# Kernel optimization log

Measured on AMD Instinct MI355X. Metric: run time of the kernel, lower is better.

The kernel has to match this reference:

```python
import jax, jax.numpy as jnp
import numpy as np

OVERSAMP = 2


def _pad_last2(x, H2, W2):
    # centered zero-pad of last two dims to (H2, W2) -- PadLast
    H, W = x.shape[-2], x.shape[-1]
    ph, pw = (H2 - H) // 2, (W2 - W) // 2
    pad = [(0, 0)] * (x.ndim - 2) + [(ph, H2 - H - ph), (pw, W2 - W - pw)]
    return jnp.pad(x, pad)


def _crop_last2(x, H, W):
    # centered crop of last two dims to (H, W) -- PadLast.adjoint
    H2, W2 = x.shape[-2], x.shape[-1]
    ph, pw = (H2 - H) // 2, (W2 - W) // 2
    return x[..., ph:ph + H, pw:pw + W]


def setup_inputs() -> dict:
    key = jax.random.key(0)
    ks = jax.random.split(key, 6)
    A, C, H, W = 5, 12, 256, 256
    Hp, Wp = OVERSAMP * H, OVERSAMP * W
    x_r = jax.random.normal(ks[0], (A, H, W), dtype=jnp.float32)
    x_i = jax.random.normal(ks[1], (A, H, W), dtype=jnp.float32)
    mps_r = jax.random.normal(ks[2], (C, H, W), dtype=jnp.float32) * 0.1
    mps_i = jax.random.normal(ks[3], (C, H, W), dtype=jnp.float32) * 0.1
    kern_r = jax.random.normal(ks[4], (A, A, Hp, Wp), dtype=jnp.float32) * 0.1
    kern_i = jax.random.normal(ks[5], (A, A, Hp, Wp), dtype=jnp.float32) * 0.1
    return {"x_r": x_r, "x_i": x_i, "mps_r": mps_r, "mps_i": mps_i,
            "kern_r": kern_r, "kern_i": kern_i}


def reference(x_r, x_i, mps_r, mps_i, kern_r, kern_i):
    # Toeplitz normal operator AHA_func: x [A,H,W] -> [A,H,W]
    x = jax.lax.complex(x_r, x_i)          # [A,H,W]
    mps = jax.lax.complex(mps_r, mps_i)    # [C,H,W]
    kernels = jax.lax.complex(kern_r, kern_i)  # [Aout,Ain,2H,2W]
    A, H, W = x.shape
    Hp, Wp = kernels.shape[-2], kernels.shape[-1]
    # coil modulation: x[None,:] * mps[:,None] -> [C,A,H,W]
    cx = mps[:, None, :, :] * x[None, :, :, :]
    cx = _pad_last2(cx, Hp, Wp)            # [C,A,2H,2W]
    Fx = jnp.fft.fftn(cx, axes=(-2, -1), norm='ortho')
    # Fx[:,None] [C,1,Ain,2H,2W] * kernels [Aout,Ain,2H,2W] -> [C,Aout,Ain,2H,2W]
    y = (OVERSAMP ** 2) * jnp.fft.ifftn(Fx[:, None, ...] * kernels,
                                        axes=(-2, -1), norm='ortho')
    y = jnp.sum(y, axis=2)                 # sum over Ain -> [C,Aout,2H,2W]
    y = _crop_last2(y, H, W)               # [C,A,H,W]
    y = y * jnp.conj(mps)[:, None, :, :]
    return jnp.sum(y, axis=0)              # [A,H,W]
```

## Files before the change

### kernel.cpp

```cpp
#include <hip/hip_runtime.h>
#include <cstddef>

#define A_  5
#define C_  12
#define RPG (C_ * A_)
#define TWO_PI 6.28318530717958647692f
#define NPAD 596

__device__ float2 g_bufA[RPG * 512 * 256];
__device__ float2 g_bufB[RPG * 512 * 256];

__device__ __forceinline__ int P5(int i) { return i + 5 * (i >> 5); }
__device__ __forceinline__ int PT(int i) { return i + (i >> 3); }

__device__ __forceinline__ void build_tab(float2* tab, int t) {
    #pragma unroll
    for (int q = 0; q < 2; ++q) {
        int k = t + q * 128;
        float s, c;
        __sincosf(-TWO_PI * (float)k * (1.0f / 512.0f), &s, &c);
        tab[PT(k)] = make_float2(c, s);
    }
}

template<int DIR>
__device__ __forceinline__ float2 cmulw(float2 v, float2 w) {
    float cv = w.x, sv = (DIR < 0) ? w.y : -w.y;
    return make_float2(v.x * cv - v.y * sv, v.x * sv + v.y * cv);
}

template<int DIR, int NB>
__device__ void fftB(float (*AR)[NPAD], float (*AI)[NPAD],
                     float (*BR)[NPAD], float (*BI)[NPAD],
                     const float2* tab, int t) {
    float (*sR)[NPAD] = AR; float (*sI)[NPAD] = AI;
    float (*dR)[NPAD] = BR; float (*dI)[NPAD] = BI;
    int Ns = 1;
    #pragma unroll
    for (int s = 0; s < 4; ++s) {
        __syncthreads();
        int m = t & (Ns - 1);
        int e1 = m << (7 - 2 * s);
        float2 w1 = tab[PT(e1)], w2 = tab[PT(2 * e1)];
        float2 w3 = make_float2(w1.x * w2.x - w1.y * w2.y,
                                w1.x * w2.y + w1.y * w2.x);
        int i0 = P5(t), i1 = P5(t + 128), i2 = P5(t + 256), i3 = P5(t + 384);
        int idxD = ((t & ~(Ns - 1)) << 2) | m;
        int o0 = P5(idxD), o1 = P5(idxD + Ns);
        int o2 = P5(idxD + 2 * Ns), o3 = P5(idxD + 3 * Ns);
        #pragma unroll
        for (int b = 0; b < NB; ++b) {
            float2 v0 = make_float2(sR[b][i0], sI[b][i0]);
            float2 v1 = cmulw<DIR>(make_float2(sR[b][i1], sI[b][i1]), w1);
            float2 v2 = cmulw<DIR>(make_float2(sR[b][i2], sI[b][i2]), w2);
            float2 v3 = cmulw<DIR>(make_float2(sR[b][i3], sI[b][i3]), w3);
            float2 t0 = make_float2(v0.x + v2.x, v0.y + v2.y);
            float2 t1 = make_float2(v0.x - v2.x, v0.y - v2.y);
            float2 t2 = make_float2(v1.x + v3.x, v1.y + v3.y);
            float2 t3 = make_float2(v1.x - v3.x, v1.y - v3.y);
            float2 y0 = make_float2(t0.x + t2.x, t0.y + t2.y);
            float2 y2 = make_float2(t0.x - t2.x, t0.y - t2.y);
            float2 y1, y3;
            if (DIR < 0) {
                y1 = make_float2(t1.x + t3.y, t1.y - t3.x);
                y3 = make_float2(t1.x - t3.y, t1.y + t3.x);
            } else {
                y1 = make_float2(t1.x - t3.y, t1.y + t3.x);
                y3 = make_float2(t1.x + t3.y, t1.y - t3.x);
            }
            dR[b][o0] = y0.x; dI[b][o0] = y0.y;
            dR[b][o1] = y1.x; dI[b][o1] = y1.y;
            dR[b][o2] = y2.x; dI[b][o2] = y2.y;
            dR[b][o3] = y3.x; dI[b][o3] = y3.y;
        }
        { auto tp = sR; sR = dR; dR = tp; }
        { auto tp = sI; sI = dI; dI = tp; }
        Ns <<= 2;
    }
    __syncthreads();
    #pragma unroll
    for (int q = 0; q < 2; ++q) {
        int j2 = t + q * 128;
        float2 w = tab[PT(j2)];
        int i0 = P5(j2), i1 = P5(j2 + 256);
        #pragma unroll
        for (int b = 0; b < NB; ++b) {
            float2 v0 = make_float2(sR[b][i0], sI[b][i0]);
            float2 tw = cmulw<DIR>(make_float2(sR[b][i1], sI[b][i1]), w);
            dR[b][i0] = v0.x + tw.x; dI[b][i0] = v0.y + tw.y;
            dR[b][i1] = v0.x - tw.x; dI[b][i1] = v0.y - tw.y;
        }
    }
    __syncthreads();
}

__global__ void k_zero(float* __restrict__ out, int n) {
    int i = blockIdx.x * 256 + threadIdx.x;
    int stride = gridDim.x * 256;
    for (; i < n; i += stride) out[i] = 0.f;
}

__global__ void __launch_bounds__(128) k_fft1c(const float* __restrict__ xr_,
        const float* __restrict__ xi_, const float* __restrict__ mr_,
        const float* __restrict__ mi_) {
    __shared__ float AR[4][NPAD], AI[4][NPAD], BR[4][NPAD], BI[4][NPAD];
    __shared__ float2 tab[288];
    int bid = blockIdx.x;
    int ca = bid >> 6;
    int x0 = (bid & 63) << 2;
    int coil = ca / A_, a = ca % A_;
    int t = threadIdx.x;
    build_tab(tab, t);
    int xc = t & 3, yo = t >> 2;
    int xcol = x0 + xc;
    const float* xr = xr_ + a * 65536;
    const float* xi = xi_ + a * 65536;
    const float* mr = mr_ + coil * 65536;
    const float* mi = mi_ + coil * 65536;
    #pragma unroll
    for (int r = 0; r < 4; ++r) {
        int z = yo + 32 * r;
        AR[xc][P5(z)] = 0.f;        AI[xc][P5(z)] = 0.f;
        AR[xc][P5(384 + z)] = 0.f;  AI[xc][P5(384 + z)] = 0.f;
    }
    #pragma unroll
    for (int r = 0; r < 8; ++r) {
        int y = yo + 32 * r;
        int idx = y * 256 + xcol;
        float xrv = xr[idx], xiv = xi[idx], mrv = mr[idx], miv = mi[idx];
        int p = P5(128 + y);
        AR[xc][p] = xrv * mrv - xiv * miv;
        AI[xc][p] = xrv * miv + xiv * mrv;
    }
    fftB<-1, 4>(AR, AI, BR, BI, tab, t);
    float2* o = g_bufA + (size_t)ca * 131072 + x0 + xc;
    #pragma unroll
    for (int rr = 0; rr < 16; ++rr) {
        int ky = yo + 32 * rr;
        int p = P5(ky);
        o[(size_t)ky * 256] = make_float2(BR[xc][p], BI[xc][p]);
    }
}

#define KLOAD(KR, KI, q) { _Pragma("unroll")                                   \
    for (int m = 0; m < 25; ++m) {                                             \
        size_t idx = ((size_t)m << 18) + kyBase + (size_t)(t + (q) * 128);     \
        KR[m] = kr[idx]; KI[m] = ki[idx]; } }

#define MIXQ(KR, KI, q) { int p = P5(t + (q) * 128);                           \
    float fr[5], fi[5];                                                        \
    _Pragma("unroll") for (int ain = 0; ain < 5; ++ain) {                      \
        fr[ain] = F1R[ain][p]; fi[ain] = F1I[ain][p]; }                        \
    _Pragma("unroll") for (int ao = 0; ao < 5; ++ao) {                         \
        float gr = 0.f, gi = 0.f;                                              \
        _Pragma("unroll") for (int ain = 0; ain < 5; ++ain) {                  \
            float kre = KR[ao * 5 + ain], kim = KI[ao * 5 + ain];              \
            gr += kre * fr[ain] - kim * fi[ain];                               \
            gi += kre * fi[ain] + kim * fr[ain]; }                             \
        F1R[ao][p] = scale * gr; F1I[ao][p] = scale * gi; } }

__global__ void __launch_bounds__(128) k_colfmc(const float* __restrict__ kr,
                                                const float* __restrict__ ki) {
    __shared__ float F0R[5][NPAD], F0I[5][NPAD], F1R[5][NPAD], F1I[5][NPAD];
    __shared__ float2 tab[288];
    int b = blockIdx.x;
    int xcd = b & 7, s = b >> 3;
    int v = s / 96, wv = s % 96;
    int u = xcd + (v << 3);
    int coil = wv % C_;
    int ky = (u << 3) + (wv / C_);
    int t = threadIdx.x;
    build_tab(tab, t);
    const float2* bA = g_bufA + (size_t)(coil * A_) * 131072 + ((size_t)ky << 8);
    float4 row[5];
    #pragma unroll
    for (int ain = 0; ain < 5; ++ain)
        row[ain] = ((const float4*)(bA + (size_t)ain * 131072))[t];
    size_t kyBase = (size_t)ky << 9;
    float kRa[25], kIa[25], kRb[25], kIb[25];
    KLOAD(kRa, kIa, 0);
    #pragma unroll
    for (int ain = 0; ain < 5; ++ain) {
        F0R[ain][P5(t)] = 0.f;        F0I[ain][P5(t)] = 0.f;
        F0R[ain][P5(t + 384)] = 0.f;  F0I[ain][P5(t + 384)] = 0.f;
        int p0 = P5(128 + 2 * t), p1 = P5(129 + 2 * t);
        F0R[ain][p0] = row[ain].x; F0I[ain][p0] = row[ain].y;
        F0R[ain][p1] = row[ain].z; F0I[ain][p1] = row[ain].w;
    }
    fftB<-1, 5>(F0R, F0I, F1R, F1I, tab, t);
    const float scale = 4.0f / 262144.0f;
    KLOAD(kRb, kIb, 1);
    MIXQ(kRa, kIa, 0);
    KLOAD(kRa, kIa, 2);
    MIXQ(kRb, kIb, 1);
    KLOAD(kRb, kIb, 3);
    MIXQ(kRa, kIa, 2);
    MIXQ(kRb, kIb, 3);
    fftB<1, 5>(F1R, F1I, F0R, F0I, tab, t);
    #pragma unroll
    for (int ao = 0; ao < 5; ++ao) {
        int p0 = P5(128 + 2 * t), p1 = P5(129 + 2 * t);
        float4 vv = make_float4(F0R[ao][p0], F0I[ao][p0],
                                F0R[ao][p1], F0I[ao][p1]);
        ((float4*)(g_bufB + (size_t)(coil * A_ + ao) * 131072 +
                   ((size_t)ky << 8)))[t] = vv;
    }
}

__global__ void __launch_bounds__(128) k_outfr(const float* __restrict__ mr_,
        const float* __restrict__ mi_, float* __restrict__ out, int outFloats) {
    __shared__ float AR[4][NPAD], AI[4][NPAD], BR[4][NPAD], BI[4][NPAD];
    __shared__ float2 tab[288];
    int bid = blockIdx.x;
    int a = bid >> 8;
    int x0 = ((bid >> 2) & 63) << 2;
    int cg = bid & 3;
    int t = threadIdx.x;
    build_tab(tab, t);
    int xc = t & 3, yo = t >> 2;
    int xcol = x0 + xc;
    float accR[8], accI[8];
    #pragma unroll
    for (int r = 0; r < 8; ++r) { accR[r] = 0.f; accI[r] = 0.f; }
    for (int cc = 0; cc < 3; ++cc) {
        int c = cg * 3 + cc;
        const float2* src = g_bufB + (size_t)(c * A_ + a) * 131072 + xcol;
        #pragma unroll
        for (int rr = 0; rr < 16; ++rr) {
            int ky = yo + 32 * rr;
            float2 vv = src[(size_t)ky * 256];
            int p = P5(ky);
            AR[xc][p] = vv.x; AI[xc][p] = vv.y;
        }
        fftB<1, 4>(AR, AI, BR, BI, tab, t);
        const float* mr = mr_ + c * 65536;
        const float* mi = mi_ + c * 65536;
        #pragma unroll
        for (int rr = 0; rr < 8; ++rr) {
            int y = yo + 32 * rr;
            int p = P5(128 + y);
            float vx = BR[xc][p], vy = BI[xc][p];
            int idx = y * 256 + xcol;
            float mrv = mr[idx], miv = mi[idx];
            accR[rr] += vx * mrv + vy * miv;
            accI[rr] += vy * mrv - vx * miv;
        }
    }
    #pragma unroll
    for (int rr = 0; rr < 8; ++rr) {
        int y = yo + 32 * rr;
        size_t r0 = (size_t)a * 65536 + (size_t)y * 256 + xcol;
        size_t i0 = 327680 + r0;
        if (r0 < (size_t)outFloats) atomicAdd(&out[r0], accR[rr]);
        if (i0 < (size_t)outFloats) atomicAdd(&out[i0], accI[rr]);
    }
}

extern "C" void kernel_launch(void* const* d_in, const int* in_sizes, int n_in,
                              void* d_out, int out_size, void* d_ws, size_t ws_size,
                              hipStream_t stream) {
    const float* xr = (const float*)d_in[0];
    const float* xi = (const float*)d_in[1];
    const float* mr = (const float*)d_in[2];
    const float* mi = (const float*)d_in[3];
    const float* kr = (const float*)d_in[4];
    const float* ki = (const float*)d_in[5];
    float* out = (float*)d_out;
    (void)d_ws; (void)ws_size; (void)n_in; (void)in_sizes;

    int nz = out_size < 655360 ? out_size : 655360;
    k_zero  <<<256, 256, 0, stream>>>(out, nz);
    k_fft1c <<<RPG * 64, 128, 0, stream>>>(xr, xi, mr, mi);
    k_colfmc<<<C_ * 512, 128, 0, stream>>>(kr, ki);
    k_outfr <<<A_ * 256, 128, 0, stream>>>(mr, mi, out, out_size);
}
```

Baseline: 313.3 us.

## Use wavefront-local radix-8 FFT in mix kernel and double threads per block

The middle kernel's row FFTs become a per-wavefront 512-point radix-8 transform held in registers. Each of five wavefronts does one channel and exchanges data through LDS with only s_waitcnt instead of block barriers. The kernel-matrix mixing now loads kernel values inline across 256 threads instead of prefetching into large register arrays. The column FFT kernels move from 128 to 256 threads, each thread handling two of the four columns, to raise parallelism and cut per-thread work. This trades fewer barriers and less register pressure for twiddles computed by recurrence, which lose some accuracy, and for less overlap of the kernel loads.

```diff
diff --git a/kernel.cpp b/kernel.cpp
--- a/kernel.cpp
+++ b/kernel.cpp
@@ -13,13 +13,11 @@
 __device__ __forceinline__ int P5(int i) { return i + 5 * (i >> 5); }
 __device__ __forceinline__ int PT(int i) { return i + (i >> 3); }
 
-__device__ __forceinline__ void build_tab(float2* tab, int t) {
-    #pragma unroll
-    for (int q = 0; q < 2; ++q) {
-        int k = t + q * 128;
+__device__ __forceinline__ void build_tab256(float2* tab, int t) {
+    if (t < 256) {
         float s, c;
-        __sincosf(-TWO_PI * (float)k * (1.0f / 512.0f), &s, &c);
-        tab[PT(k)] = make_float2(c, s);
+        __sincosf(-TWO_PI * (float)t * (1.0f / 512.0f), &s, &c);
+        tab[PT(t)] = make_float2(c, s);
     }
 }
 
@@ -29,27 +27,100 @@
     return make_float2(v.x * cv - v.y * sv, v.x * sv + v.y * cv);
 }
 
-template<int DIR, int NB>
-__device__ void fftB(float (*AR)[NPAD], float (*AI)[NPAD],
-                     float (*BR)[NPAD], float (*BI)[NPAD],
-                     const float2* tab, int t) {
+template<int DIR>
+__device__ __forceinline__ void dft8(float* xr, float* xi) {
+    const float S = 0.70710678118654752f;
+    float ar[4], ai[4], br[4], bi[4];
+#pragma unroll
+    for (int j = 0; j < 4; ++j) {
+        ar[j] = xr[j] + xr[j+4]; ai[j] = xi[j] + xi[j+4];
+        br[j] = xr[j] - xr[j+4]; bi[j] = xi[j] - xi[j+4];
+    }
+    float t;
+    if (DIR < 0) {
+        t = S*(br[1]+bi[1]); bi[1] = S*(bi[1]-br[1]); br[1] = t;
+        t = bi[2];           bi[2] = -br[2];          br[2] = t;
+        t = S*(bi[3]-br[3]); bi[3] = -S*(br[3]+bi[3]); br[3] = t;
+    } else {
+        t = S*(br[1]-bi[1]); bi[1] = S*(bi[1]+br[1]); br[1] = t;
+        t = -bi[2];          bi[2] = br[2];           br[2] = t;
+        t = -S*(br[3]+bi[3]); bi[3] = S*(br[3]-bi[3]); br[3] = t;
+    }
+    float c0r=ar[0]+ar[2], c0i=ai[0]+ai[2], c1r=ar[1]+ar[3], c1i=ai[1]+ai[3];
+    float d0r=ar[0]-ar[2], d0i=ai[0]-ai[2], d1r, d1i;
+    if (DIR < 0) { d1r =  ai[1]-ai[3]; d1i = -(ar[1]-ar[3]); }
+    else         { d1r = -(ai[1]-ai[3]); d1i =  ar[1]-ar[3]; }
+    xr[0]=c0r+c1r; xi[0]=c0i+c1i; xr[4]=c0r-c1r; xi[4]=c0i-c1i;
+    xr[2]=d0r+d1r; xi[2]=d0i+d1i; xr[6]=d0r-d1r; xi[6]=d0i-d1i;
+    c0r=br[0]+br[2]; c0i=bi[0]+bi[2]; c1r=br[1]+br[3]; c1i=bi[1]+bi[3];
+    d0r=br[0]-br[2]; d0i=bi[0]-bi[2];
+    if (DIR < 0) { d1r =  bi[1]-bi[3]; d1i = -(br[1]-br[3]); }
+    else         { d1r = -(bi[1]-bi[3]); d1i =  br[1]-br[3]; }
+    xr[1]=c0r+c1r; xi[1]=c0i+c1i; xr[5]=c0r-c1r; xi[5]=c0i-c1i;
+    xr[3]=d0r+d1r; xi[3]=d0i+d1i; xr[7]=d0r-d1r; xi[7]=d0i-d1i;
+}
+
+__device__ __forceinline__ void twiddle_chain(float* vr, float* vi, float ang) {
+    float s, c; __sincosf(ang, &s, &c);
+    float twr = c, twi = s;
+#pragma unroll
+    for (int d = 1; d < 8; ++d) {
+        float tr = vr[d]*twr - vi[d]*twi;
+        vi[d]    = vr[d]*twi + vi[d]*twr;
+        vr[d]    = tr;
+        float nr = twr*c - twi*s;
+        twi      = twr*s + twi*c;
+        twr      = nr;
+    }
+}
+
+template<int DIR>
+__device__ __forceinline__ void wfft512(float* vr, float* vi,
+                                        float* sre, float* sim, int lh) {
+    const float sgn = (DIR < 0) ? -1.f : 1.f;
+    dft8<DIR>(vr, vi);
+    twiddle_chain(vr, vi, sgn * (TWO_PI/512.f) * (float)lh);
+#pragma unroll
+    for (int d = 0; d < 8; ++d) { sre[72*d+lh] = vr[d]; sim[72*d+lh] = vi[d]; }
+    asm volatile("s_waitcnt lgkmcnt(0)" ::: "memory");
+    int rb = 72*(lh>>3) + (lh&7);
+#pragma unroll
+    for (int e = 0; e < 8; ++e) { vr[e] = sre[rb+8*e]; vi[e] = sim[rb+8*e]; }
+    dft8<DIR>(vr, vi);
+    twiddle_chain(vr, vi, sgn * (TWO_PI/64.f) * (float)(lh & 7));
+    int wb = 9*(lh>>3) + (lh&7);
+#pragma unroll
+    for (int h = 0; h < 8; ++h) { sre[72*h+wb] = vr[h]; sim[72*h+wb] = vi[h]; }
+    asm volatile("s_waitcnt lgkmcnt(0)" ::: "memory");
+    int rb2 = 72*(lh&7) + 9*(lh>>3);
+#pragma unroll
+    for (int f = 0; f < 8; ++f) { vr[f] = sre[rb2+f]; vi[f] = sim[rb2+f]; }
+    dft8<DIR>(vr, vi);
+}
+
+template<int DIR>
+__device__ void fftB4(float (*AR)[NPAD], float (*AI)[NPAD],
+                      float (*BR)[NPAD], float (*BI)[NPAD],
+                      const float2* tab, int t) {
+    int tt = t & 127, b0 = (t >> 7) << 1;
     float (*sR)[NPAD] = AR; float (*sI)[NPAD] = AI;
     float (*dR)[NPAD] = BR; float (*dI)[NPAD] = BI;
     int Ns = 1;
     #pragma unroll
     for (int s = 0; s < 4; ++s) {
         __syncthreads();
-        int m = t & (Ns - 1);
+        int m = tt & (Ns - 1);
         int e1 = m << (7 - 2 * s);
         float2 w1 = tab[PT(e1)], w2 = tab[PT(2 * e1)];
         float2 w3 = make_float2(w1.x * w2.x - w1.y * w2.y,
                                 w1.x * w2.y + w1.y * w2.x);
-        int i0 = P5(t), i1 = P5(t + 128), i2 = P5(t + 256), i3 = P5(t + 384);
-        int idxD = ((t & ~(Ns - 1)) << 2) | m;
+        int i0 = P5(tt), i1 = P5(tt + 128), i2 = P5(tt + 256), i3 = P5(tt + 384);
+        int idxD = ((tt & ~(Ns - 1)) << 2) | m;
         int o0 = P5(idxD), o1 = P5(idxD + Ns);
         int o2 = P5(idxD + 2 * Ns), o3 = P5(idxD + 3 * Ns);
         #pragma unroll
-        for (int b = 0; b < NB; ++b) {
+        for (int bb = 0; bb < 2; ++bb) {
+            int b = b0 + bb;
             float2 v0 = make_float2(sR[b][i0], sI[b][i0]);
             float2 v1 = cmulw<DIR>(make_float2(sR[b][i1], sI[b][i1]), w1);
             float2 v2 = cmulw<DIR>(make_float2(sR[b][i2], sI[b][i2]), w2);
@@ -80,11 +151,12 @@
     __syncthreads();
     #pragma unroll
     for (int q = 0; q < 2; ++q) {
-        int j2 = t + q * 128;
+        int j2 = tt + q * 128;
         float2 w = tab[PT(j2)];
         int i0 = P5(j2), i1 = P5(j2 + 256);
         #pragma unroll
-        for (int b = 0; b < NB; ++b) {
+        for (int bb = 0; bb < 2; ++bb) {
+            int b = b0 + bb;
             float2 v0 = make_float2(sR[b][i0], sI[b][i0]);
             float2 tw = cmulw<DIR>(make_float2(sR[b][i1], sI[b][i1]), w);
             dR[b][i0] = v0.x + tw.x; dI[b][i0] = v0.y + tw.y;
@@ -100,7 +172,7 @@
     for (; i < n; i += stride) out[i] = 0.f;
 }
 
-__global__ void __launch_bounds__(128) k_fft1c(const float* __restrict__ xr_,
+__global__ void __launch_bounds__(256) k_fft1c(const float* __restrict__ xr_,
         const float* __restrict__ xi_, const float* __restrict__ mr_,
         const float* __restrict__ mi_) {
     __shared__ float AR[4][NPAD], AI[4][NPAD], BR[4][NPAD], BI[4][NPAD];
@@ -110,7 +182,7 @@
     int x0 = (bid & 63) << 2;
     int coil = ca / A_, a = ca % A_;
     int t = threadIdx.x;
-    build_tab(tab, t);
+    build_tab256(tab, t);
     int xc = t & 3, yo = t >> 2;
     int xcol = x0 + xc;
     const float* xr = xr_ + a * 65536;
@@ -118,51 +190,34 @@
     const float* mr = mr_ + coil * 65536;
     const float* mi = mi_ + coil * 65536;
     #pragma unroll
-    for (int r = 0; r < 4; ++r) {
-        int z = yo + 32 * r;
+    for (int r = 0; r < 2; ++r) {
+        int z = yo + 64 * r;
         AR[xc][P5(z)] = 0.f;        AI[xc][P5(z)] = 0.f;
         AR[xc][P5(384 + z)] = 0.f;  AI[xc][P5(384 + z)] = 0.f;
     }
     #pragma unroll
-    for (int r = 0; r < 8; ++r) {
-        int y = yo + 32 * r;
+    for (int r = 0; r < 4; ++r) {
+        int y = yo + 64 * r;
         int idx = y * 256 + xcol;
         float xrv = xr[idx], xiv = xi[idx], mrv = mr[idx], miv = mi[idx];
         int p = P5(128 + y);
         AR[xc][p] = xrv * mrv - xiv * miv;
         AI[xc][p] = xrv * miv + xiv * mrv;
     }
-    fftB<-1, 4>(AR, AI, BR, BI, tab, t);
+    fftB4<-1>(AR, AI, BR, BI, tab, t);
     float2* o = g_bufA + (size_t)ca * 131072 + x0 + xc;
     #pragma unroll
-    for (int rr = 0; rr < 16; ++rr) {
-        int ky = yo + 32 * rr;
+    for (int rr = 0; rr < 8; ++rr) {
+        int ky = yo + 64 * rr;
         int p = P5(ky);
         o[(size_t)ky * 256] = make_float2(BR[xc][p], BI[xc][p]);
     }
 }
 
-#define KLOAD(KR, KI, q) { _Pragma("unroll")                                   \
-    for (int m = 0; m < 25; ++m) {                                             \
-        size_t idx = ((size_t)m << 18) + kyBase + (size_t)(t + (q) * 128);     \
-        KR[m] = kr[idx]; KI[m] = ki[idx]; } }
-
-#define MIXQ(KR, KI, q) { int p = P5(t + (q) * 128);                           \
-    float fr[5], fi[5];                                                        \
-    _Pragma("unroll") for (int ain = 0; ain < 5; ++ain) {                      \
-        fr[ain] = F1R[ain][p]; fi[ain] = F1I[ain][p]; }                        \
-    _Pragma("unroll") for (int ao = 0; ao < 5; ++ao) {                         \
-        float gr = 0.f, gi = 0.f;                                              \
-        _Pragma("unroll") for (int ain = 0; ain < 5; ++ain) {                  \
-            float kre = KR[ao * 5 + ain], kim = KI[ao * 5 + ain];              \
-            gr += kre * fr[ain] - kim * fi[ain];                               \
-            gi += kre * fi[ain] + kim * fr[ain]; }                             \
-        F1R[ao][p] = scale * gr; F1I[ao][p] = scale * gi; } }
-
-__global__ void __launch_bounds__(128) k_colfmc(const float* __restrict__ kr,
+__global__ void __launch_bounds__(320) k_colfmc(const float* __restrict__ kr,
                                                 const float* __restrict__ ki) {
-    __shared__ float F0R[5][NPAD], F0I[5][NPAD], F1R[5][NPAD], F1I[5][NPAD];
-    __shared__ float2 tab[288];
+    __shared__ float FRe[A_][512], FIm[A_][512];
+    __shared__ float shR[A_][576], shI[A_][576];
     int b = blockIdx.x;
     int xcd = b & 7, s = b >> 3;
     int v = s / 96, wv = s % 96;
@@ -170,44 +225,79 @@
     int coil = wv % C_;
     int ky = (u << 3) + (wv / C_);
     int t = threadIdx.x;
-    build_tab(tab, t);
-    const float2* bA = g_bufA + (size_t)(coil * A_) * 131072 + ((size_t)ky << 8);
-    float4 row[5];
-    #pragma unroll
-    for (int ain = 0; ain < 5; ++ain)
-        row[ain] = ((const float4*)(bA + (size_t)ain * 131072))[t];
-    size_t kyBase = (size_t)ky << 9;
-    float kRa[25], kIa[25], kRb[25], kIb[25];
-    KLOAD(kRa, kIa, 0);
-    #pragma unroll
-    for (int ain = 0; ain < 5; ++ain) {
-        F0R[ain][P5(t)] = 0.f;        F0I[ain][P5(t)] = 0.f;
-        F0R[ain][P5(t + 384)] = 0.f;  F0I[ain][P5(t + 384)] = 0.f;
-        int p0 = P5(128 + 2 * t), p1 = P5(129 + 2 * t);
-        F0R[ain][p0] = row[ain].x; F0I[ain][p0] = row[ain].y;
-        F0R[ain][p1] = row[ain].z; F0I[ain][p1] = row[ain].w;
-    }
-    fftB<-1, 5>(F0R, F0I, F1R, F1I, tab, t);
+    int w = t >> 6, L = t & 63;
+    int sig = ((L & 7) << 3) | (L >> 3);
+    float* sre = shR[w]; float* sim = shI[w];
+
+    {
+        const float2* row = g_bufA + (size_t)(coil * A_ + w) * 131072 +
+                            ((size_t)ky << 8);
+        float vr[8], vi[8];
+        #pragma unroll
+        for (int r = 0; r < 8; ++r) { vr[r] = 0.f; vi[r] = 0.f; }
+        #pragma unroll
+        for (int r = 2; r < 6; ++r) {
+            float2 vv = row[((r - 2) << 6) + L];
+            vr[r] = vv.x; vi[r] = vv.y;
+        }
+        wfft512<-1>(vr, vi, sre, sim, L);
+        #pragma unroll
+        for (int g = 0; g < 8; ++g) {
+            int kx = (g << 6) + sig;
+            FRe[w][kx] = vr[g]; FIm[w][kx] = vi[g];
+        }
+    }
+    __syncthreads();
+
     const float scale = 4.0f / 262144.0f;
-    KLOAD(kRb, kIb, 1);
-    MIXQ(kRa, kIa, 0);
-    KLOAD(kRa, kIa, 2);
-    MIXQ(kRb, kIb, 1);
-    KLOAD(kRb, kIb, 3);
-    MIXQ(kRa, kIa, 2);
-    MIXQ(kRb, kIb, 3);
-    fftB<1, 5>(F1R, F1I, F0R, F0I, tab, t);
-    #pragma unroll
-    for (int ao = 0; ao < 5; ++ao) {
-        int p0 = P5(128 + 2 * t), p1 = P5(129 + 2 * t);
-        float4 vv = make_float4(F0R[ao][p0], F0I[ao][p0],
-                                F0R[ao][p1], F0I[ao][p1]);
-        ((float4*)(g_bufB + (size_t)(coil * A_ + ao) * 131072 +
-                   ((size_t)ky << 8)))[t] = vv;
-    }
-}
-
-__global__ void __launch_bounds__(128) k_outfr(const float* __restrict__ mr_,
+    if (t < 256) {
+        size_t kyb = (size_t)ky << 9;
+        #pragma unroll
+        for (int h = 0; h < 2; ++h) {
+            int kx = t + (h << 8);
+            float fr[A_], fi[A_];
+            #pragma unroll
+            for (int ain = 0; ain < A_; ++ain) {
+                fr[ain] = FRe[ain][kx]; fi[ain] = FIm[ain][kx];
+            }
+            float gr[A_], gi[A_];
+            #pragma unroll
+            for (int ao = 0; ao < A_; ++ao) {
+                float ar = 0.f, ai = 0.f;
+                #pragma unroll
+                for (int ain = 0; ain < A_; ++ain) {
+                    size_t idx = ((size_t)(ao * A_ + ain) << 18) + kyb + kx;
+                    float kre = kr[idx], kim = ki[idx];
+                    ar += kre * fr[ain] - kim * fi[ain];
+                    ai += kre * fi[ain] + kim * fr[ain];
+                }
+                gr[ao] = scale * ar; gi[ao] = scale * ai;
+            }
+            #pragma unroll
+            for (int ao = 0; ao < A_; ++ao) {
+                FRe[ao][kx] = gr[ao]; FIm[ao][kx] = gi[ao];
+            }
+        }
+    }
+    __syncthreads();
+
+    {
+        float vr[8], vi[8];
+        #pragma unroll
+        for (int r = 0; r < 8; ++r) {
+            int kx = (r << 6) + sig;
+            vr[r] = FRe[w][kx]; vi[r] = FIm[w][kx];
+        }
+        wfft512<1>(vr, vi, sre, sim, sig);
+        float2* oB = g_bufB + (size_t)(coil * A_ + w) * 131072 +
+                     ((size_t)ky << 8);
+        #pragma unroll
+        for (int g = 2; g < 6; ++g)
+            oB[((g - 2) << 6) + L] = make_float2(vr[g], vi[g]);
+    }
+}
+
+__global__ void __launch_bounds__(256) k_outfr(const float* __restrict__ mr_,
         const float* __restrict__ mi_, float* __restrict__ out, int outFloats) {
     __shared__ float AR[4][NPAD], AI[4][NPAD], BR[4][NPAD], BI[4][NPAD];
     __shared__ float2 tab[288];
@@ -216,28 +306,28 @@
     int x0 = ((bid >> 2) & 63) << 2;
     int cg = bid & 3;
     int t = threadIdx.x;
-    build_tab(tab, t);
+    build_tab256(tab, t);
     int xc = t & 3, yo = t >> 2;
     int xcol = x0 + xc;
-    float accR[8], accI[8];
-    #pragma unroll
-    for (int r = 0; r < 8; ++r) { accR[r] = 0.f; accI[r] = 0.f; }
+    float accR[4], accI[4];
+    #pragma unroll
+    for (int r = 0; r < 4; ++r) { accR[r] = 0.f; accI[r] = 0.f; }
     for (int cc = 0; cc < 3; ++cc) {
         int c = cg * 3 + cc;
         const float2* src = g_bufB + (size_t)(c * A_ + a) * 131072 + xcol;
         #pragma unroll
-        for (int rr = 0; rr < 16; ++rr) {
-            int ky = yo + 32 * rr;
+        for (int rr = 0; rr < 8; ++rr) {
+            int ky = yo + 64 * rr;
             float2 vv = src[(size_t)ky * 256];
             int p = P5(ky);
             AR[xc][p] = vv.x; AI[xc][p] = vv.y;
         }
-        fftB<1, 4>(AR, AI, BR, BI, tab, t);
+        fftB4<1>(AR, AI, BR, BI, tab, t);
         const float* mr = mr_ + c * 65536;
         const float* mi = mi_ + c * 65536;
         #pragma unroll
-        for (int rr = 0; rr < 8; ++rr) {
-            int y = yo + 32 * rr;
+        for (int rr = 0; rr < 4; ++rr) {
+            int y = yo + 64 * rr;
             int p = P5(128 + y);
             float vx = BR[xc][p], vy = BI[xc][p];
             int idx = y * 256 + xcol;
@@ -247,8 +337,8 @@
         }
     }
     #pragma unroll
-    for (int rr = 0; rr < 8; ++rr) {
-        int y = yo + 32 * rr;
+    for (int rr = 0; rr < 4; ++rr) {
+        int y = yo + 64 * rr;
         size_t r0 = (size_t)a * 65536 + (size_t)y * 256 + xcol;
         size_t i0 = 327680 + r0;
         if (r0 < (size_t)outFloats) atomicAdd(&out[r0], accR[rr]);
@@ -270,7 +360,7 @@
 
     int nz = out_size < 655360 ? out_size : 655360;
     k_zero  <<<256, 256, 0, stream>>>(out, nz);
-    k_fft1c <<<RPG * 64, 128, 0, stream>>>(xr, xi, mr, mi);
-    k_colfmc<<<C_ * 512, 128, 0, stream>>>(kr, ki);
-    k_outfr <<<A_ * 256, 128, 0, stream>>>(mr, mi, out, out_size);
-}
+    k_fft1c <<<RPG * 64, 256, 0, stream>>>(xr, xi, mr, mi);
+    k_colfmc<<<C_ * 512, 320, 0, stream>>>(kr, ki);
+    k_outfr <<<A_ * 256, 256, 0, stream>>>(mr, mi, out, out_size);
+}
```

After: 350.8 us. +12.0%, slower.

## Process FFT rows one channel at a time to shrink LDS footprint

Applied to the files above, without the earlier changes.

The column FFT/kernel-multiply kernel now transforms each input channel separately through a single-row LDS buffer and keeps the spectra in registers, then computes and inverse-transforms each output channel in turn. This cuts shared memory from five rows of four buffers to one row each, and drops the double-buffered 50-register kernel prefetch, so more blocks can be resident per CU. In exchange it serializes ten small FFTs with their barriers and loses the overlap of kernel loads with FFT work, since kernel values are now loaded just before use.

```diff
diff --git a/kernel.cpp b/kernel.cpp
--- a/kernel.cpp
+++ b/kernel.cpp
@@ -142,26 +142,9 @@
     }
 }
 
-#define KLOAD(KR, KI, q) { _Pragma("unroll")                                   \
-    for (int m = 0; m < 25; ++m) {                                             \
-        size_t idx = ((size_t)m << 18) + kyBase + (size_t)(t + (q) * 128);     \
-        KR[m] = kr[idx]; KI[m] = ki[idx]; } }
-
-#define MIXQ(KR, KI, q) { int p = P5(t + (q) * 128);                           \
-    float fr[5], fi[5];                                                        \
-    _Pragma("unroll") for (int ain = 0; ain < 5; ++ain) {                      \
-        fr[ain] = F1R[ain][p]; fi[ain] = F1I[ain][p]; }                        \
-    _Pragma("unroll") for (int ao = 0; ao < 5; ++ao) {                         \
-        float gr = 0.f, gi = 0.f;                                              \
-        _Pragma("unroll") for (int ain = 0; ain < 5; ++ain) {                  \
-            float kre = KR[ao * 5 + ain], kim = KI[ao * 5 + ain];              \
-            gr += kre * fr[ain] - kim * fi[ain];                               \
-            gi += kre * fi[ain] + kim * fr[ain]; }                             \
-        F1R[ao][p] = scale * gr; F1I[ao][p] = scale * gi; } }
-
 __global__ void __launch_bounds__(128) k_colfmc(const float* __restrict__ kr,
                                                 const float* __restrict__ ki) {
-    __shared__ float F0R[5][NPAD], F0I[5][NPAD], F1R[5][NPAD], F1I[5][NPAD];
+    __shared__ float AR[1][NPAD], AI[1][NPAD], BR[1][NPAD], BI[1][NPAD];
     __shared__ float2 tab[288];
     int b = blockIdx.x;
     int xcd = b & 7, s = b >> 3;
@@ -171,37 +154,51 @@
     int ky = (u << 3) + (wv / C_);
     int t = threadIdx.x;
     build_tab(tab, t);
+
+    float FrR[A_][4], FrI[A_][4];
+
     const float2* bA = g_bufA + (size_t)(coil * A_) * 131072 + ((size_t)ky << 8);
-    float4 row[5];
-    #pragma unroll
-    for (int ain = 0; ain < 5; ++ain)
-        row[ain] = ((const float4*)(bA + (size_t)ain * 131072))[t];
-    size_t kyBase = (size_t)ky << 9;
-    float kRa[25], kIa[25], kRb[25], kIb[25];
-    KLOAD(kRa, kIa, 0);
-    #pragma unroll
-    for (int ain = 0; ain < 5; ++ain) {
-        F0R[ain][P5(t)] = 0.f;        F0I[ain][P5(t)] = 0.f;
-        F0R[ain][P5(t + 384)] = 0.f;  F0I[ain][P5(t + 384)] = 0.f;
+    for (int ain = 0; ain < A_; ++ain) {
+        float4 row = ((const float4*)(bA + (size_t)ain * 131072))[t];
+        AR[0][P5(t)] = 0.f;        AI[0][P5(t)] = 0.f;
+        AR[0][P5(t + 384)] = 0.f;  AI[0][P5(t + 384)] = 0.f;
         int p0 = P5(128 + 2 * t), p1 = P5(129 + 2 * t);
-        F0R[ain][p0] = row[ain].x; F0I[ain][p0] = row[ain].y;
-        F0R[ain][p1] = row[ain].z; F0I[ain][p1] = row[ain].w;
-    }
-    fftB<-1, 5>(F0R, F0I, F1R, F1I, tab, t);
+        AR[0][p0] = row.x; AI[0][p0] = row.y;
+        AR[0][p1] = row.z; AI[0][p1] = row.w;
+        fftB<-1, 1>(AR, AI, BR, BI, tab, t);
+        #pragma unroll
+        for (int q = 0; q < 4; ++q) {
+            int p = P5(t + q * 128);
+            FrR[ain][q] = BR[0][p];
+            FrI[ain][q] = BI[0][p];
+        }
+    }
+
     const float scale = 4.0f / 262144.0f;
-    KLOAD(kRb, kIb, 1);
-    MIXQ(kRa, kIa, 0);
-    KLOAD(kRa, kIa, 2);
-    MIXQ(kRb, kIb, 1);
-    KLOAD(kRb, kIb, 3);
-    MIXQ(kRa, kIa, 2);
-    MIXQ(kRb, kIb, 3);
-    fftB<1, 5>(F1R, F1I, F0R, F0I, tab, t);
-    #pragma unroll
-    for (int ao = 0; ao < 5; ++ao) {
+    size_t kyb = ((size_t)ky << 9) + t;
+    for (int ao = 0; ao < A_; ++ao) {
+        #pragma unroll
+        for (int q = 0; q < 4; ++q) {
+            int kx = t + q * 128;
+            float kre[A_], kim[A_];
+            #pragma unroll
+            for (int ain = 0; ain < A_; ++ain) {
+                size_t idx = ((size_t)(ao * A_ + ain) << 18) + kyb + (size_t)(q * 128);
+                kre[ain] = kr[idx]; kim[ain] = ki[idx];
+            }
+            float gr = 0.f, gi = 0.f;
+            #pragma unroll
+            for (int ain = 0; ain < A_; ++ain) {
+                gr += kre[ain] * FrR[ain][q] - kim[ain] * FrI[ain][q];
+                gi += kre[ain] * FrI[ain][q] + kim[ain] * FrR[ain][q];
+            }
+            int p = P5(kx);
+            AR[0][p] = scale * gr;
+            AI[0][p] = scale * gi;
+        }
+        fftB<1, 1>(AR, AI, BR, BI, tab, t);
         int p0 = P5(128 + 2 * t), p1 = P5(129 + 2 * t);
-        float4 vv = make_float4(F0R[ao][p0], F0I[ao][p0],
-                                F0R[ao][p1], F0I[ao][p1]);
+        float4 vv = make_float4(BR[0][p0], BI[0][p0], BR[0][p1], BI[0][p1]);
         ((float4*)(g_bufB + (size_t)(coil * A_ + ao) * 131072 +
                    ((size_t)ky << 8)))[t] = vv;
     }
```

Result: faster. 296.7 us (-5.3%).
